# Kernel tuning notes

Measured on AMD Instinct MI355X. Metric: run time of the kernel, lower is better.

The kernel has to match this reference:

```python
import jax, jax.numpy as jnp
import numpy as np

B, T, D, H = 4, 1024, 1024, 16  # batch, seq, model dim (named head_size in source), n_heads


def setup_inputs() -> dict:
    key = jax.random.key(0)
    ks = jax.random.split(key, 12)
    s = 0.02
    x = jax.random.normal(ks[0], (B, T, D), jnp.float32)
    x1 = jax.random.normal(ks[1], (1,), jnp.float32)  # unused by module
    x2 = jax.random.normal(ks[2], (1,), jnp.float32)  # unused by module
    # bool mask, True = masked out; causal upper-triangular as typical usage
    attn_mask = jnp.triu(jnp.ones((T, T), dtype=bool), k=1)
    Wk = jax.random.normal(ks[3], (D, D), jnp.float32) * s
    bk = jax.random.normal(ks[4], (D,), jnp.float32) * s
    Wq = jax.random.normal(ks[5], (D, D), jnp.float32) * s
    bq = jax.random.normal(ks[6], (D,), jnp.float32) * s
    Wv = jax.random.normal(ks[7], (D, D), jnp.float32) * s
    bv = jax.random.normal(ks[8], (D,), jnp.float32) * s
    Wp = jax.random.normal(ks[9], (D, D), jnp.float32) * s
    bp = jax.random.normal(ks[10], (D,), jnp.float32) * s
    return {"x": x, "x1": x1, "x2": x2, "attn_mask": attn_mask,
            "Wk": Wk, "bk": bk, "Wq": Wq, "bq": bq,
            "Wv": Wv, "bv": bv, "Wp": Wp, "bp": bp}


def reference(x, x1, x2, attn_mask, Wk, bk, Wq, bq, Wv, bv, Wp, bp):
    b, t, c = x.shape
    n_heads = H
    hd = c // n_heads
    # torch nn.Linear: y = x @ W.T + b
    k = (x @ Wk.T + bk).reshape(b, t, n_heads, hd)
    q = (x @ Wq.T + bq).reshape(b, t, n_heads, hd)
    v = (x @ Wv.T + bv).reshape(b, t, n_heads, hd)
    scores = jnp.einsum('bkhi,bqhi->bkqh', k, q)  # [B,T(k),T(q),H]
    # mask BEFORE scaling (as in source; -inf is scale-invariant)
    scores = jnp.where(attn_mask[None, :t, :t, None], -jnp.inf, scores)
    scores = scores / jnp.sqrt(jnp.asarray(c, scores.dtype))  # scale by full model dim (source quirk)
    weights = jax.nn.softmax(scores, axis=2)  # softmax over QUERY axis (source quirk)
    out = jnp.einsum('bkqh,bqhj->bkhj', weights, v).reshape(b, t, c)
    out = out @ Wp.T + bp  # dropout p=0 -> identity
    return (out, weights)
```

## Files before the change

kernel.cpp:

```cpp
#include <hip/hip_runtime.h>
#include <cstdint>


typedef __bf16 bf16x8 __attribute__((ext_vector_type(8)));
typedef float  f32x4  __attribute__((ext_vector_type(4)));
typedef unsigned int u32x4 __attribute__((ext_vector_type(4)));
using u16 = unsigned short;
using u32 = unsigned int;

__device__ __forceinline__ float bf2f(u16 u) {
  union { u32 u; float f; } x; x.u = ((u32)u) << 16; return x.f;
}
__device__ __forceinline__ u16 f2bf(float f) {
  union { float f; u32 u; } x; x.f = f;
  u32 u = x.u;
  return (u16)((u + 0x7fffu + ((u >> 16) & 1u)) >> 16);
}

__device__ __forceinline__ void storeC(float* p, float v) { *p = v; }
__device__ __forceinline__ void storeC(u16* p, float v)   { *p = f2bf(v); }

#define GLL(g, s) __builtin_amdgcn_global_load_lds(                      \
    (const __attribute__((address_space(1))) u32*)(g),                   \
    (__attribute__((address_space(3))) u32*)(s), 16, 0, 0)

__global__ __launch_bounds__(256) void cvt_all(const float4* __restrict__ x,
                                               const float4* __restrict__ wk,
                                               const float4* __restrict__ wq,
                                               const float4* __restrict__ wv,
                                               const float4* __restrict__ wp,
                                               uint2* __restrict__ out,
                                               const float* __restrict__ bkp,
                                               const float* __restrict__ bqp,
                                               float* __restrict__ bqkv) {
  if (blockIdx.x >= 8192) {
    int t2 = (blockIdx.x - 8192) * 256 + threadIdx.x;
    const float* s = (t2 < 1024) ? bkp : bqp;
    bqkv[t2] = s[t2 & 1023];
    return;
  }
  int i = blockIdx.x * 256 + threadIdx.x;
  const float4* src; int off;
  if (i < 1048576) { src = x; off = i; }
  else {
    int j = i - 1048576; int w = j >> 18; off = j & 262143;
    src = (w == 0) ? wk : (w == 1) ? wq : (w == 2) ? wv : wp;
  }
  float4 v = src[off];
  uint2 o;
  o.x = (u32)f2bf(v.x) | ((u32)f2bf(v.y) << 16);
  o.y = (u32)f2bf(v.z) | ((u32)f2bf(v.w) << 16);
  out[i] = o;
}

__global__ __launch_bounds__(256) void gemm_qkvt(
    const u16* __restrict__ xb, const u16* __restrict__ wkb,
    const float* __restrict__ bkq, const float* __restrict__ bv,
    u16* __restrict__ kq, u16* __restrict__ vt)
{
  const int z  = blockIdx.z;
  const int n0 = blockIdx.x * 128;
  const u16 *A, *B; u16* C; const float* bias;
  int m0; bool rowBias;
  if (z < 2) {
    m0 = blockIdx.y * 128;
    A = xb; B = wkb + z * 1048576; C = kq + (size_t)z * 4194304;
    bias = bkq + z * 1024; rowBias = false;
  } else {
    const int b = blockIdx.y >> 3;
    m0 = (blockIdx.y & 7) * 128;
    A = wkb + 2 * 1048576; B = xb + (size_t)b * 1048576; C = vt + (size_t)b * 1048576;
    bias = bv; rowBias = true;
  }

  __shared__ __align__(16) u16 As[128 * 32];
  __shared__ __align__(16) u16 Bs[128 * 32];

  const int t    = threadIdx.x;
  const int wave = t >> 6;
  const int lane = t & 63;

  const int r0 = (wave * 2 + 0) * 16 + (lane >> 2);
  const int r1 = (wave * 2 + 1) * 16 + (lane >> 2);
  const int cl = (lane & 3) * 8;
  const u16* aG0 = A + (size_t)(m0 + r0) * 1024 + cl;
  const u16* aG1 = A + (size_t)(m0 + r1) * 1024 + cl;
  const u16* bG0 = B + (size_t)(n0 + r0) * 1024 + cl;
  const u16* bG1 = B + (size_t)(n0 + r1) * 1024 + cl;
  u16* asD0 = As + (wave * 2 + 0) * 512;
  u16* asD1 = As + (wave * 2 + 1) * 512;
  u16* bsD0 = Bs + (wave * 2 + 0) * 512;
  u16* bsD1 = Bs + (wave * 2 + 1) * 512;

  const int wm = (wave >> 1) << 6;
  const int wn = (wave & 1) << 6;
  const int lr = lane & 15;
  const int lk = (lane >> 4) << 3;

  f32x4 acc[4][4];
  const f32x4 fzero = {0.f, 0.f, 0.f, 0.f};
#pragma unroll
  for (int i = 0; i < 4; i++)
#pragma unroll
    for (int j = 0; j < 4; j++) acc[i][j] = fzero;

  for (int k0 = 0; k0 < 1024; k0 += 32) {
    __syncthreads();
    GLL(aG0 + k0, asD0);
    GLL(aG1 + k0, asD1);
    GLL(bG0 + k0, bsD0);
    GLL(bG1 + k0, bsD1);
    __syncthreads();

    bf16x8 af[4], bf[4];
#pragma unroll
    for (int mi = 0; mi < 4; mi++)
      af[mi] = *(const bf16x8*)&As[(wm + mi * 16 + lr) * 32 + lk];
#pragma unroll
    for (int ni = 0; ni < 4; ni++)
      bf[ni] = *(const bf16x8*)&Bs[(wn + ni * 16 + lr) * 32 + lk];
#pragma unroll
    for (int mi = 0; mi < 4; mi++)
#pragma unroll
      for (int ni = 0; ni < 4; ni++)
        acc[mi][ni] = __builtin_amdgcn_mfma_f32_16x16x32_bf16(af[mi], bf[ni], acc[mi][ni], 0, 0, 0);
  }

  const int cr = (lane >> 4) << 2;
  const int cc = lane & 15;
#pragma unroll
  for (int mi = 0; mi < 4; mi++) {
#pragma unroll
    for (int ni = 0; ni < 4; ni++) {
      int gn = n0 + wn + ni * 16 + cc;
      float bcol = rowBias ? 0.f : bias[gn];
      int gm = m0 + wm + mi * 16 + cr;
#pragma unroll
      for (int r = 0; r < 4; r++) {
        float badd = rowBias ? bias[gm + r] : bcol;
        C[(size_t)(gm + r) * 1024 + gn] = f2bf(acc[mi][ni][r] + badd);
      }
    }
  }
}

template <typename CT>
__global__ __launch_bounds__(256) void gemm_nt(
    const u16* __restrict__ A, const u16* __restrict__ B,
    const float* __restrict__ bias, CT* __restrict__ C,
    int M, int N, int K, int lda, int ldb, int ldc,
    int nH, long long sAb, long long sAh, long long sBb, long long sBh,
    long long sCb, long long sCh, float alpha, int biasStrideH)
{
  const int m0 = blockIdx.y * 128;
  const int n0 = blockIdx.x * 128;

  int z = blockIdx.z;
  int bb = z / nH, hh = z % nH;
  A += bb * sAb + hh * sAh;
  B += bb * sBb + hh * sBh;
  C += bb * sCb + hh * sCh;

  __shared__ __align__(16) u16 As[128 * 32];
  __shared__ __align__(16) u16 Bs[128 * 32];

  const int t    = threadIdx.x;
  const int wave = t >> 6;
  const int lane = t & 63;

  const int r0 = (wave * 2 + 0) * 16 + (lane >> 2);
  const int r1 = (wave * 2 + 1) * 16 + (lane >> 2);
  const int cl = (lane & 3) * 8;
  const u16* aG0 = A + (size_t)(m0 + r0) * lda + cl;
  const u16* aG1 = A + (size_t)(m0 + r1) * lda + cl;
  const u16* bG0 = B + (size_t)(n0 + r0) * ldb + cl;
  const u16* bG1 = B + (size_t)(n0 + r1) * ldb + cl;
  u16* asD0 = As + (wave * 2 + 0) * 512;
  u16* asD1 = As + (wave * 2 + 1) * 512;
  u16* bsD0 = Bs + (wave * 2 + 0) * 512;
  u16* bsD1 = Bs + (wave * 2 + 1) * 512;

  const int wm = (wave >> 1) << 6;
  const int wn = (wave & 1) << 6;
  const int lr = lane & 15;
  const int lk = (lane >> 4) << 3;

  f32x4 acc[4][4];
  const f32x4 fzero = {0.f, 0.f, 0.f, 0.f};
#pragma unroll
  for (int i = 0; i < 4; i++)
#pragma unroll
    for (int j = 0; j < 4; j++) acc[i][j] = fzero;

  for (int k0 = 0; k0 < K; k0 += 32) {
    __syncthreads();
    GLL(aG0 + k0, asD0);
    GLL(aG1 + k0, asD1);
    GLL(bG0 + k0, bsD0);
    GLL(bG1 + k0, bsD1);
    __syncthreads();

    bf16x8 af[4], bf[4];
#pragma unroll
    for (int mi = 0; mi < 4; mi++)
      af[mi] = *(const bf16x8*)&As[(wm + mi * 16 + lr) * 32 + lk];
#pragma unroll
    for (int ni = 0; ni < 4; ni++)
      bf[ni] = *(const bf16x8*)&Bs[(wn + ni * 16 + lr) * 32 + lk];
#pragma unroll
    for (int mi = 0; mi < 4; mi++)
#pragma unroll
      for (int ni = 0; ni < 4; ni++)
        acc[mi][ni] = __builtin_amdgcn_mfma_f32_16x16x32_bf16(af[mi], bf[ni], acc[mi][ni], 0, 0, 0);
  }

  const int cr = (lane >> 4) << 2;
  const int cc = lane & 15;
#pragma unroll
  for (int mi = 0; mi < 4; mi++) {
#pragma unroll
    for (int ni = 0; ni < 4; ni++) {
      int gn = n0 + wn + ni * 16 + cc;
      if (gn >= N) continue;
      float bv = bias ? bias[biasStrideH * hh + gn] : 0.f;
      int gm = m0 + wm + mi * 16 + cr;
#pragma unroll
      for (int r = 0; r < 4; r++) {
        float v = acc[mi][ni][r] * alpha + bv;
        storeC(&C[(size_t)(gm + r) * ldc + gn], v);
      }
    }
  }
}

__global__ __launch_bounds__(256, 2) void fused_attn(
    const u16* __restrict__ kq,
    const u16* __restrict__ vt,
    u16* __restrict__ sc, u16* __restrict__ attn, float* __restrict__ lbuf)
{
  const int xx = blockIdx.x, yy = blockIdx.y;
  int kbv = (xx + yy) & 7;
  if (yy & 32) kbv = 7 - kbv;
  const int kb = kbv;
  const int bh = yy;
  const int b  = bh >> 4, h = bh & 15;
  const int k0 = kb << 7;

  __shared__ __align__(16) u16 Kl[128 * 72];
  __shared__ __align__(16) u16 QV[128 * 72];
  __shared__ __align__(16) u16 Pl[128 * 136];
  __shared__ float l_sm[2][128];

  const int t    = threadIdx.x;
  const int wave = t >> 6, lane = t & 63;
  const int wm = (wave >> 1) << 6, wn = (wave & 1) << 6;
  const int lr = lane & 15, lk = (lane >> 4) << 3;
  const int cr = (lane >> 4) << 2, cc = lane & 15;

  {
    const int r = t >> 1, cb = (t & 1) << 5;
    const u16* g = kq + (size_t)(b * 1024 + k0 + r) * 1024 + h * 64 + cb;
    u16* d = Kl + r * 72 + cb;
#pragma unroll
    for (int i = 0; i < 4; i++)
      *(uint4*)(d + i * 8) = *(const uint4*)(g + i * 8);
  }

  const u16* qbase = kq + 4194304 + (size_t)(b * 1024) * 1024 + h * 64;
  const u16* vbase = vt + (size_t)(bh * 64) * 1024;

  f32x4 oacc[2][4];
  const f32x4 fz = {0.f, 0.f, 0.f, 0.f};
#pragma unroll
  for (int i = 0; i < 2; i++)
#pragma unroll
    for (int j = 0; j < 4; j++) oacc[i][j] = fz;
  float lsum[4][4] = {};

  const int qr = t >> 1, qcb = (t & 1) << 5;
  const int vr = t >> 2, vcb = (t & 3) << 5;

  for (int tq = 0; tq <= kb; tq++) {
    const int q0 = tq << 7;
    uint4 qreg[4], vreg[4];
    const u16* qg = qbase + (size_t)(q0 + qr) * 1024 + qcb;
    const u16* vg = vbase + (size_t)vr * 1024 + q0 + vcb;
#pragma unroll
    for (int i = 0; i < 4; i++) qreg[i] = *(const uint4*)(qg + i * 8);
#pragma unroll
    for (int i = 0; i < 4; i++) vreg[i] = *(const uint4*)(vg + i * 8);

    __syncthreads();
    {
      u16* d = QV + qr * 72 + qcb;
#pragma unroll
      for (int i = 0; i < 4; i++) *(uint4*)(d + i * 8) = qreg[i];
    }
    __syncthreads();

    f32x4 sacc[4][4];
#pragma unroll
    for (int i = 0; i < 4; i++)
#pragma unroll
      for (int j = 0; j < 4; j++) sacc[i][j] = fz;
#pragma unroll
    for (int ks = 0; ks < 2; ks++) {
      bf16x8 af[4], bf[4];
#pragma unroll
      for (int mi = 0; mi < 4; mi++)
        af[mi] = *(const bf16x8*)&Kl[(wm + mi * 16 + lr) * 72 + ks * 32 + lk];
#pragma unroll
      for (int ni = 0; ni < 4; ni++)
        bf[ni] = *(const bf16x8*)&QV[(wn + ni * 16 + lr) * 72 + ks * 32 + lk];
#pragma unroll
      for (int mi = 0; mi < 4; mi++)
#pragma unroll
        for (int ni = 0; ni < 4; ni++)
          sacc[mi][ni] = __builtin_amdgcn_mfma_f32_16x16x32_bf16(af[mi], bf[ni], sacc[mi][ni], 0, 0, 0);
    }
    __syncthreads();

#pragma unroll
    for (int mi = 0; mi < 4; mi++) {
#pragma unroll
      for (int ni = 0; ni < 4; ni++) {
        const int col = wn + ni * 16 + cc;
#pragma unroll
        for (int r = 0; r < 4; r++) {
          const int row = wm + mi * 16 + cr + r;
          bool valid = (q0 + col) <= (k0 + row);
          float e = valid ? __expf(sacc[mi][ni][r] * 0.03125f) : 0.f;
          lsum[mi][r] += e;
          Pl[row * 136 + col] = f2bf(e);
        }
      }
    }
    {
      u16* d = QV + vr * 136 + vcb;
#pragma unroll
      for (int i = 0; i < 4; i++) *(uint4*)(d + i * 8) = vreg[i];
    }
    __syncthreads();

#pragma unroll
    for (int ks = 0; ks < 4; ks++) {
      bf16x8 pa[2], vb[4];
#pragma unroll
      for (int mi = 0; mi < 2; mi++)
        pa[mi] = *(const bf16x8*)&Pl[(wave * 32 + mi * 16 + lr) * 136 + ks * 32 + lk];
#pragma unroll
      for (int ni = 0; ni < 4; ni++)
        vb[ni] = *(const bf16x8*)&QV[(ni * 16 + lr) * 136 + ks * 32 + lk];
#pragma unroll
      for (int mi = 0; mi < 2; mi++)
#pragma unroll
        for (int ni = 0; ni < 4; ni++)
          oacc[mi][ni] = __builtin_amdgcn_mfma_f32_16x16x32_bf16(pa[mi], vb[ni], oacc[mi][ni], 0, 0, 0);
    }
    {
      const int rr = t >> 4, cp = (t & 15) << 3;
      u16* g = sc + ((size_t)bh << 20) + (size_t)(k0 + rr) * 1024 + q0 + cp;
      const u16* s = Pl + rr * 136 + cp;
#pragma unroll
      for (int i = 0; i < 8; i++) {
        u32x4 v = *(const u32x4*)(s + i * 16 * 136);
        __builtin_nontemporal_store(v, (u32x4*)(g + (size_t)(i * 16) * 1024));
      }
    }
  }

#pragma unroll
  for (int mi = 0; mi < 4; mi++)
#pragma unroll
    for (int r = 0; r < 4; r++) {
      float v = lsum[mi][r];
#pragma unroll
      for (int o = 1; o < 16; o <<= 1) v += __shfl_xor(v, o, 64);
      lsum[mi][r] = v;
    }
  __syncthreads();
  if ((lane & 15) == 0) {
#pragma unroll
    for (int mi = 0; mi < 4; mi++)
#pragma unroll
      for (int r = 0; r < 4; r++)
        l_sm[wave & 1][wm + mi * 16 + cr + r] = lsum[mi][r];
  }
  __syncthreads();
  if (t < 128)
    lbuf[(size_t)bh * 1024 + k0 + t] = l_sm[0][t] + l_sm[1][t];

#pragma unroll
  for (int mi = 0; mi < 2; mi++) {
#pragma unroll
    for (int r = 0; r < 4; r++) {
      const int row = wave * 32 + mi * 16 + cr + r;
      const float rinv = 1.f / (l_sm[0][row] + l_sm[1][row]);
#pragma unroll
      for (int ni = 0; ni < 4; ni++)
        attn[(size_t)(b * 1024 + k0 + row) * 1024 + h * 64 + ni * 16 + cc] =
            f2bf(oacc[mi][ni][r] * rinv);
    }
  }
}

__global__ __launch_bounds__(1024) void expand_norm(const u16* __restrict__ sw,
                                                    const float* __restrict__ lbuf,
                                                    float* __restrict__ out_w) {
  __shared__ u32 lds[16 * 577];

  const int bk   = blockIdx.x;
  const int b    = bk >> 10, k = bk & 1023;
  const int w    = threadIdx.x >> 6;
  const int lane = threadIdx.x & 63;
  const int qb   = lane << 4;

  const float rinv = 1.f / lbuf[(size_t)(b * 16 + w) * 1024 + k];
  const u16* row = sw + (((size_t)(b * 16 + w)) << 20) + ((size_t)k << 10);

  union { u32x4 d; u16 s[8]; } a0, a1;
  if (qb <= k) {
    a0.d = __builtin_nontemporal_load((const u32x4*)(row + qb));
    a1.d = __builtin_nontemporal_load((const u32x4*)(row + qb + 8));
  } else {
    a0.d = (u32x4){0, 0, 0, 0};
    a1.d = (u32x4){0, 0, 0, 0};
  }

  u16 outp[16];
#pragma unroll
  for (int j = 0; j < 16; j++) {
    u16 raw = (j < 8) ? a0.s[j] : a1.s[j - 8];
    float e = ((qb + j) <= k) ? bf2f(raw) * rinv : 0.f;
    outp[j] = f2bf(e);
  }

  u32* run = &lds[w * 577 + lane * 9];
#pragma unroll
  for (int j = 0; j < 8; j++) run[j] = (u32)outp[2 * j] | ((u32)outp[2 * j + 1] << 16);
  __syncthreads();

  const int t = threadIdx.x;
  f32x4* o = (f32x4*)(out_w + ((size_t)bk << 14));
#pragma unroll
  for (int p = 0; p < 4; p++) {
    const int q    = p * 256 + (t >> 2);
    const int Lr   = q >> 4;
    const int pr   = (q & 15) >> 1;
    const int half = (q & 1) << 4;
    f32x4 v;
#pragma unroll
    for (int j = 0; j < 4; j++) {
      const int hh = (t & 3) * 4 + j;
      u32 packed = lds[hh * 577 + Lr * 9 + pr];
      v[j] = bf2f((u16)(packed >> half));
    }
    __builtin_nontemporal_store(v, o + p * 1024 + t);
  }
}

extern "C" void kernel_launch(void* const* d_in, const int* in_sizes, int n_in,
                              void* d_out, int out_size, void* d_ws, size_t ws_size,
                              hipStream_t stream) {
  const float* x  = (const float*)d_in[0];
  const float* Wk = (const float*)d_in[4];
  const float* bk = (const float*)d_in[5];
  const float* Wq = (const float*)d_in[6];
  const float* bq = (const float*)d_in[7];
  const float* Wv = (const float*)d_in[8];
  const float* bv = (const float*)d_in[9];
  const float* Wp = (const float*)d_in[10];
  const float* bp = (const float*)d_in[11];

  float* out   = (float*)d_out;
  float* out_w = out + 4194304;

  u16* ws   = (u16*)d_ws;
  u16* xb   = ws;
  u16* wkb  = xb  + 4194304;
  u16* kbuf = wkb + 4194304;
  u16* vt   = kbuf + 12582912;
  u16* attn = vt   + 4194304;
  u16* sc   = attn + 4194304;
  float* bqkv = (float*)(sc + 67108864);
  float* lbuf = bqkv + 3072;

  cvt_all<<<8200, 256, 0, stream>>>((const float4*)x, (const float4*)Wk, (const float4*)Wq,
                                    (const float4*)Wv, (const float4*)Wp, (uint2*)ws,
                                    bk, bq, bqkv);

  gemm_qkvt<<<dim3(8, 32, 3), 256, 0, stream>>>(xb, wkb, bqkv, bv, kbuf, vt);

  fused_attn<<<dim3(8, 64), 256, 0, stream>>>(kbuf, vt, sc, attn, lbuf);

  expand_norm<<<4096, 1024, 0, stream>>>(sc, lbuf, out_w);

  gemm_nt<float><<<dim3(8, 32, 1), 256, 0, stream>>>(
      attn, wkb + 3145728, bp, out, 4096, 1024, 1024, 1024, 1024, 1024,
      1, 0, 0, 0, 0, 0, 0, 1.0f, 0);
}
```

Before: 466.8 us.

## Merge output projection GEMM and weight expansion into one launch

Combines the final projection GEMM and the softmax-weight expansion kernel into a single launch. The first 256 blocks compute the projection tile while the remaining blocks expand normalized weights, and the expand path now uses 256 threads that each handle four heads. This removes one kernel launch and lets the compute-bound GEMM overlap with the bandwidth-bound weight writeout. The input conversion also switches to nontemporal loads. In exchange, shared memory is sized for the larger expand buffer, which may lower GEMM occupancy, and the smaller expand blocks run more store iterations each.

```diff
diff --git a/kernel.cpp b/kernel.cpp
--- a/kernel.cpp
+++ b/kernel.cpp
@@ -17,18 +17,15 @@
   return (u16)((u + 0x7fffu + ((u >> 16) & 1u)) >> 16);
 }
 
-__device__ __forceinline__ void storeC(float* p, float v) { *p = v; }
-__device__ __forceinline__ void storeC(u16* p, float v)   { *p = f2bf(v); }
-
 #define GLL(g, s) __builtin_amdgcn_global_load_lds(                      \
     (const __attribute__((address_space(1))) u32*)(g),                   \
     (__attribute__((address_space(3))) u32*)(s), 16, 0, 0)
 
-__global__ __launch_bounds__(256) void cvt_all(const float4* __restrict__ x,
-                                               const float4* __restrict__ wk,
-                                               const float4* __restrict__ wq,
-                                               const float4* __restrict__ wv,
-                                               const float4* __restrict__ wp,
+__global__ __launch_bounds__(256) void cvt_all(const float* __restrict__ x,
+                                               const float* __restrict__ wk,
+                                               const float* __restrict__ wq,
+                                               const float* __restrict__ wv,
+                                               const float* __restrict__ wp,
                                                uint2* __restrict__ out,
                                                const float* __restrict__ bkp,
                                                const float* __restrict__ bqp,
@@ -40,16 +37,16 @@
     return;
   }
   int i = blockIdx.x * 256 + threadIdx.x;
-  const float4* src; int off;
+  const float* src; int off;
   if (i < 1048576) { src = x; off = i; }
   else {
     int j = i - 1048576; int w = j >> 18; off = j & 262143;
     src = (w == 0) ? wk : (w == 1) ? wq : (w == 2) ? wv : wp;
   }
-  float4 v = src[off];
+  f32x4 v = __builtin_nontemporal_load((const f32x4*)(src + off * 4));
   uint2 o;
-  o.x = (u32)f2bf(v.x) | ((u32)f2bf(v.y) << 16);
-  o.y = (u32)f2bf(v.z) | ((u32)f2bf(v.w) << 16);
+  o.x = (u32)f2bf(v[0]) | ((u32)f2bf(v[1]) << 16);
+  o.y = (u32)f2bf(v[2]) | ((u32)f2bf(v[3]) << 16);
   out[i] = o;
 }
 
@@ -144,95 +141,6 @@
   }
 }
 
-template <typename CT>
-__global__ __launch_bounds__(256) void gemm_nt(
-    const u16* __restrict__ A, const u16* __restrict__ B,
-    const float* __restrict__ bias, CT* __restrict__ C,
-    int M, int N, int K, int lda, int ldb, int ldc,
-    int nH, long long sAb, long long sAh, long long sBb, long long sBh,
-    long long sCb, long long sCh, float alpha, int biasStrideH)
-{
-  const int m0 = blockIdx.y * 128;
-  const int n0 = blockIdx.x * 128;
-
-  int z = blockIdx.z;
-  int bb = z / nH, hh = z % nH;
-  A += bb * sAb + hh * sAh;
-  B += bb * sBb + hh * sBh;
-  C += bb * sCb + hh * sCh;
-
-  __shared__ __align__(16) u16 As[128 * 32];
-  __shared__ __align__(16) u16 Bs[128 * 32];
-
-  const int t    = threadIdx.x;
-  const int wave = t >> 6;
-  const int lane = t & 63;
-
-  const int r0 = (wave * 2 + 0) * 16 + (lane >> 2);
-  const int r1 = (wave * 2 + 1) * 16 + (lane >> 2);
-  const int cl = (lane & 3) * 8;
-  const u16* aG0 = A + (size_t)(m0 + r0) * lda + cl;
-  const u16* aG1 = A + (size_t)(m0 + r1) * lda + cl;
-  const u16* bG0 = B + (size_t)(n0 + r0) * ldb + cl;
-  const u16* bG1 = B + (size_t)(n0 + r1) * ldb + cl;
-  u16* asD0 = As + (wave * 2 + 0) * 512;
-  u16* asD1 = As + (wave * 2 + 1) * 512;
-  u16* bsD0 = Bs + (wave * 2 + 0) * 512;
-  u16* bsD1 = Bs + (wave * 2 + 1) * 512;
-
-  const int wm = (wave >> 1) << 6;
-  const int wn = (wave & 1) << 6;
-  const int lr = lane & 15;
-  const int lk = (lane >> 4) << 3;
-
-  f32x4 acc[4][4];
-  const f32x4 fzero = {0.f, 0.f, 0.f, 0.f};
-#pragma unroll
-  for (int i = 0; i < 4; i++)
-#pragma unroll
-    for (int j = 0; j < 4; j++) acc[i][j] = fzero;
-
-  for (int k0 = 0; k0 < K; k0 += 32) {
-    __syncthreads();
-    GLL(aG0 + k0, asD0);
-    GLL(aG1 + k0, asD1);
-    GLL(bG0 + k0, bsD0);
-    GLL(bG1 + k0, bsD1);
-    __syncthreads();
-
-    bf16x8 af[4], bf[4];
-#pragma unroll
-    for (int mi = 0; mi < 4; mi++)
-      af[mi] = *(const bf16x8*)&As[(wm + mi * 16 + lr) * 32 + lk];
-#pragma unroll
-    for (int ni = 0; ni < 4; ni++)
-      bf[ni] = *(const bf16x8*)&Bs[(wn + ni * 16 + lr) * 32 + lk];
-#pragma unroll
-    for (int mi = 0; mi < 4; mi++)
-#pragma unroll
-      for (int ni = 0; ni < 4; ni++)
-        acc[mi][ni] = __builtin_amdgcn_mfma_f32_16x16x32_bf16(af[mi], bf[ni], acc[mi][ni], 0, 0, 0);
-  }
-
-  const int cr = (lane >> 4) << 2;
-  const int cc = lane & 15;
-#pragma unroll
-  for (int mi = 0; mi < 4; mi++) {
-#pragma unroll
-    for (int ni = 0; ni < 4; ni++) {
-      int gn = n0 + wn + ni * 16 + cc;
-      if (gn >= N) continue;
-      float bv = bias ? bias[biasStrideH * hh + gn] : 0.f;
-      int gm = m0 + wm + mi * 16 + cr;
-#pragma unroll
-      for (int r = 0; r < 4; r++) {
-        float v = acc[mi][ni][r] * alpha + bv;
-        storeC(&C[(size_t)(gm + r) * ldc + gn], v);
-      }
-    }
-  }
-}
-
 __global__ __launch_bounds__(256, 2) void fused_attn(
     const u16* __restrict__ kq,
     const u16* __restrict__ vt,
@@ -404,47 +312,128 @@
   }
 }
 
-__global__ __launch_bounds__(1024) void expand_norm(const u16* __restrict__ sw,
-                                                    const float* __restrict__ lbuf,
-                                                    float* __restrict__ out_w) {
-  __shared__ u32 lds[16 * 577];
-
-  const int bk   = blockIdx.x;
+__global__ __launch_bounds__(256) void expand_proj(
+    const u16* __restrict__ sw, const float* __restrict__ lbuf, float* __restrict__ out_w,
+    const u16* __restrict__ A, const u16* __restrict__ Bw,
+    const float* __restrict__ bias, float* __restrict__ Cout)
+{
+  __shared__ __align__(16) u32 shm[16 * 577];
+
+  if (blockIdx.x < 256) {
+    const int bx = blockIdx.x;
+    const int m0 = (bx >> 3) * 128;
+    const int n0 = (bx & 7) * 128;
+
+    u16* AsB = (u16*)shm;
+    u16* BsB = AsB + 4096;
+
+    const int t    = threadIdx.x;
+    const int wave = t >> 6;
+    const int lane = t & 63;
+
+    const int r0 = (wave * 2 + 0) * 16 + (lane >> 2);
+    const int r1 = (wave * 2 + 1) * 16 + (lane >> 2);
+    const int cl = (lane & 3) * 8;
+    const u16* aG0 = A + (size_t)(m0 + r0) * 1024 + cl;
+    const u16* aG1 = A + (size_t)(m0 + r1) * 1024 + cl;
+    const u16* bG0 = Bw + (size_t)(n0 + r0) * 1024 + cl;
+    const u16* bG1 = Bw + (size_t)(n0 + r1) * 1024 + cl;
+    u16* asD0 = AsB + (wave * 2 + 0) * 512;
+    u16* asD1 = AsB + (wave * 2 + 1) * 512;
+    u16* bsD0 = BsB + (wave * 2 + 0) * 512;
+    u16* bsD1 = BsB + (wave * 2 + 1) * 512;
+
+    const int wm = (wave >> 1) << 6;
+    const int wn = (wave & 1) << 6;
+    const int lr = lane & 15;
+    const int lk = (lane >> 4) << 3;
+
+    f32x4 acc[4][4];
+    const f32x4 fzero = {0.f, 0.f, 0.f, 0.f};
+#pragma unroll
+    for (int i = 0; i < 4; i++)
+#pragma unroll
+      for (int j = 0; j < 4; j++) acc[i][j] = fzero;
+
+    for (int k0 = 0; k0 < 1024; k0 += 32) {
+      __syncthreads();
+      GLL(aG0 + k0, asD0);
+      GLL(aG1 + k0, asD1);
+      GLL(bG0 + k0, bsD0);
+      GLL(bG1 + k0, bsD1);
+      __syncthreads();
+
+      bf16x8 af[4], bf[4];
+#pragma unroll
+      for (int mi = 0; mi < 4; mi++)
+        af[mi] = *(const bf16x8*)&AsB[(wm + mi * 16 + lr) * 32 + lk];
+#pragma unroll
+      for (int ni = 0; ni < 4; ni++)
+        bf[ni] = *(const bf16x8*)&BsB[(wn + ni * 16 + lr) * 32 + lk];
+#pragma unroll
+      for (int mi = 0; mi < 4; mi++)
+#pragma unroll
+        for (int ni = 0; ni < 4; ni++)
+          acc[mi][ni] = __builtin_amdgcn_mfma_f32_16x16x32_bf16(af[mi], bf[ni], acc[mi][ni], 0, 0, 0);
+    }
+
+    const int cr = (lane >> 4) << 2;
+    const int cc = lane & 15;
+#pragma unroll
+    for (int mi = 0; mi < 4; mi++) {
+#pragma unroll
+      for (int ni = 0; ni < 4; ni++) {
+        int gn = n0 + wn + ni * 16 + cc;
+        float bv = bias[gn];
+        int gm = m0 + wm + mi * 16 + cr;
+#pragma unroll
+        for (int r = 0; r < 4; r++)
+          Cout[(size_t)(gm + r) * 1024 + gn] = acc[mi][ni][r] + bv;
+      }
+    }
+    return;
+  }
+
+  const int bk   = blockIdx.x - 256;
   const int b    = bk >> 10, k = bk & 1023;
-  const int w    = threadIdx.x >> 6;
-  const int lane = threadIdx.x & 63;
+  const int t    = threadIdx.x;
+  const int wave = t >> 6;
+  const int lane = t & 63;
   const int qb   = lane << 4;
 
-  const float rinv = 1.f / lbuf[(size_t)(b * 16 + w) * 1024 + k];
-  const u16* row = sw + (((size_t)(b * 16 + w)) << 20) + ((size_t)k << 10);
-
-  union { u32x4 d; u16 s[8]; } a0, a1;
-  if (qb <= k) {
-    a0.d = __builtin_nontemporal_load((const u32x4*)(row + qb));
-    a1.d = __builtin_nontemporal_load((const u32x4*)(row + qb + 8));
-  } else {
-    a0.d = (u32x4){0, 0, 0, 0};
-    a1.d = (u32x4){0, 0, 0, 0};
-  }
-
-  u16 outp[16];
-#pragma unroll
-  for (int j = 0; j < 16; j++) {
-    u16 raw = (j < 8) ? a0.s[j] : a1.s[j - 8];
-    float e = ((qb + j) <= k) ? bf2f(raw) * rinv : 0.f;
-    outp[j] = f2bf(e);
-  }
-
-  u32* run = &lds[w * 577 + lane * 9];
-#pragma unroll
-  for (int j = 0; j < 8; j++) run[j] = (u32)outp[2 * j] | ((u32)outp[2 * j + 1] << 16);
+#pragma unroll
+  for (int i = 0; i < 4; i++) {
+    const int h = wave * 4 + i;
+    const float rinv = 1.f / lbuf[(size_t)(b * 16 + h) * 1024 + k];
+    const u16* row = sw + (((size_t)(b * 16 + h)) << 20) + ((size_t)k << 10);
+
+    union { u32x4 d; u16 s[8]; } a0, a1;
+    if (qb <= k) {
+      a0.d = __builtin_nontemporal_load((const u32x4*)(row + qb));
+      a1.d = __builtin_nontemporal_load((const u32x4*)(row + qb + 8));
+    } else {
+      a0.d = (u32x4){0, 0, 0, 0};
+      a1.d = (u32x4){0, 0, 0, 0};
+    }
+
+    u16 outp[16];
+#pragma unroll
+    for (int j = 0; j < 16; j++) {
+      u16 raw = (j < 8) ? a0.s[j] : a1.s[j - 8];
+      float e = ((qb + j) <= k) ? bf2f(raw) * rinv : 0.f;
+      outp[j] = f2bf(e);
+    }
+
+    u32* run = &shm[h * 577 + lane * 9];
+#pragma unroll
+    for (int j = 0; j < 8; j++) run[j] = (u32)outp[2 * j] | ((u32)outp[2 * j + 1] << 16);
+  }
   __syncthreads();
 
-  const int t = threadIdx.x;
   f32x4* o = (f32x4*)(out_w + ((size_t)bk << 14));
 #pragma unroll
-  for (int p = 0; p < 4; p++) {
-    const int q    = p * 256 + (t >> 2);
+  for (int p = 0; p < 16; p++) {
+    const int q    = p * 64 + (t >> 2);
     const int Lr   = q >> 4;
     const int pr   = (q & 15) >> 1;
     const int half = (q & 1) << 4;
@@ -452,10 +441,10 @@
 #pragma unroll
     for (int j = 0; j < 4; j++) {
       const int hh = (t & 3) * 4 + j;
-      u32 packed = lds[hh * 577 + Lr * 9 + pr];
+      u32 packed = shm[hh * 577 + Lr * 9 + pr];
       v[j] = bf2f((u16)(packed >> half));
     }
-    __builtin_nontemporal_store(v, o + p * 1024 + t);
+    __builtin_nontemporal_store(v, o + p * 256 + t);
   }
 }
 
@@ -485,17 +474,12 @@
   float* bqkv = (float*)(sc + 67108864);
   float* lbuf = bqkv + 3072;
 
-  cvt_all<<<8200, 256, 0, stream>>>((const float4*)x, (const float4*)Wk, (const float4*)Wq,
-                                    (const float4*)Wv, (const float4*)Wp, (uint2*)ws,
-                                    bk, bq, bqkv);
+  cvt_all<<<8200, 256, 0, stream>>>(x, Wk, Wq, Wv, Wp, (uint2*)ws, bk, bq, bqkv);
 
   gemm_qkvt<<<dim3(8, 32, 3), 256, 0, stream>>>(xb, wkb, bqkv, bv, kbuf, vt);
 
   fused_attn<<<dim3(8, 64), 256, 0, stream>>>(kbuf, vt, sc, attn, lbuf);
 
-  expand_norm<<<4096, 1024, 0, stream>>>(sc, lbuf, out_w);
-
-  gemm_nt<float><<<dim3(8, 32, 1), 256, 0, stream>>>(
-      attn, wkb + 3145728, bp, out, 4096, 1024, 1024, 1024, 1024, 1024,
-      1, 0, 0, 0, 0, 0, 0, 1.0f, 0);
-}
+  expand_proj<<<4352, 256, 0, stream>>>(sc, lbuf, out_w,
+                                        attn, wkb + 3145728, bp, out);
+}
```

After: 461.2 us. About the same (-1.2%).
